# Kernel tuning notes

Hardware: AMD Instinct MI355X
Metric: run time of the kernel (lower is better)

The kernel has to match this reference:

```python
import jax, jax.numpy as jnp
import numpy as np

B, N, D, H = 4, 2048, 1024, 16
DH = D // H

def setup_inputs() -> dict:
    key = jax.random.key(0)
    kx, kqkv, ko = jax.random.split(key, 3)
    x = jax.random.normal(kx, (B, N, D), dtype=jnp.float32)
    # torch Linear weights: [out, in]; scale like default init
    W_qkv = jax.random.normal(kqkv, (3 * D, D), dtype=jnp.float32) * (1.0 / np.sqrt(D))
    W_out = jax.random.normal(ko, (D, D), dtype=jnp.float32) * (1.0 / np.sqrt(D))
    return {"x": x, "W_qkv": W_qkv, "W_out": W_out}

def reference(x, W_qkv, W_out):
    Bk, Nk, C = x.shape
    qkv = jnp.einsum('bnc,oc->bno', x, W_qkv)  # [B,N,3D]
    qkv = qkv.reshape(Bk, Nk, 3, H, DH).transpose(2, 0, 3, 1, 4)  # [3,B,H,N,DH]
    q, k, v = qkv[0], qkv[1], qkv[2]
    att = jnp.einsum('bhnd,bhmd->bhnm', q, k) * (1.0 / np.sqrt(DH))
    mask = jnp.triu(jnp.ones((Nk, Nk), dtype=bool), k=1)  # True above diagonal
    att = jnp.where(mask, -jnp.inf, att)
    att = jax.nn.softmax(att, axis=-1)
    y = jnp.einsum('bhnm,bhmd->bhnd', att, v)  # [B,H,N,DH]
    y = y.transpose(0, 2, 1, 3).reshape(Bk, Nk, C)
    return jnp.einsum('bnc,oc->bno', y, W_out)
```

## Files before the change

### kernel.cpp

```cpp
#include <hip/hip_runtime.h>
#include <hip/hip_bf16.h>
#include <stdint.h>

#define Bb 4
#define Nn 2048
#define Dd 1024
#define Hh 16
#define DHd 64
#define Mm (Bb*Nn)
#define D3 (3*Dd)

typedef unsigned short u16;
typedef unsigned int u32;
typedef __attribute__((ext_vector_type(8))) short bf16x8;
typedef __attribute__((ext_vector_type(4))) float f32x4;
typedef __attribute__((ext_vector_type(16))) float f32x16;
typedef __attribute__((ext_vector_type(4))) unsigned int u32x4;

__device__ __forceinline__ u16 f2bf(float f) {
    unsigned int u = __float_as_uint(f);
    u = (u + 0x7FFFu + ((u >> 16) & 1u)) >> 16;
    return (u16)u;
}

__device__ __forceinline__ u32 cvtpk_bf16(float lo, float hi) {
    u32 r;
    asm("v_cvt_pk_bf16_f32 %0, %1, %2" : "=v"(r) : "v"(lo), "v"(hi));
    return r;
}

__device__ __forceinline__ float fexp2(float x) {
    float r;
    asm("v_exp_f32 %0, %1" : "=v"(r) : "v"(x));
    return r;
}

#define GLOAD16(g, l)                                                          \
    __builtin_amdgcn_global_load_lds(                                          \
        (const __attribute__((address_space(1))) unsigned int*)(g),            \
        (__attribute__((address_space(3))) unsigned int*)(l), 16, 0, 0)

__global__ void cvt_all(const float* __restrict__ x, const float* __restrict__ wqkv,
                        const float* __restrict__ wout, u16* __restrict__ xb,
                        u16* __restrict__ wqkvb, u16* __restrict__ woutb, float s) {
    const int A4 = Mm * Dd / 4;
    const int B4 = D3 * Dd / 4;
    const int C4 = Dd * Dd / 4;
    const int QCUT = Dd * Dd / 4;
    const int total = A4 + B4 + C4;
    int i = blockIdx.x * blockDim.x + threadIdx.x;
    const int stride = gridDim.x * blockDim.x;
    for (; i < total; i += stride) {
        const float* src; u16* dst; int j; float sc = 1.f;
        if (i < A4) { src = x; dst = xb; j = i; }
        else if (i < A4 + B4) { j = i - A4; src = wqkv; dst = wqkvb; if (j < QCUT) sc = s; }
        else { j = i - A4 - B4; src = wout; dst = woutb; }
        float4 v = ((const float4*)src)[j];
        u16 o0 = f2bf(v.x * sc), o1 = f2bf(v.y * sc), o2 = f2bf(v.z * sc), o3 = f2bf(v.w * sc);
        ((uint2*)dst)[j] = make_uint2((u32)o0 | ((u32)o1 << 16), (u32)o2 | ((u32)o3 << 16));
    }
}

template<int OUT_F32>
__global__ __launch_bounds__(256) void gemm_bt(const u16* __restrict__ A,
                                               const u16* __restrict__ Bm,
                                               void* __restrict__ C,
                                               int M, int Nout, int K) {
    __shared__ u16 As[128 * 64];
    __shared__ u16 Bs[128 * 64];
    const int t = threadIdx.x;
    const int lane = t & 63;
    const int w = t >> 6;
    const int wr = w >> 1, wc = w & 1;
    const int l15 = lane & 15, l4 = lane >> 4;

    const int gx = gridDim.x;
    const int linear = blockIdx.y * gx + blockIdx.x;
    const int cpx = (gx * gridDim.y) >> 3;
    const int tile = (linear & 7) * cpx + (linear >> 3);
    const int m0 = (tile / gx) * 128;
    const int n0 = (tile % gx) * 128;

    f32x4 acc[4][4] = {};

    for (int k0 = 0; k0 < K; k0 += 64) {
        __syncthreads();
#pragma unroll
        for (int i = 0; i < 4; i++) {
            int chunk = i * 256 + t;
            int row = chunk >> 3;
            int csw = ((chunk & 7) ^ (row & 7)) << 3;
            GLOAD16(A + (size_t)(m0 + row) * K + k0 + csw, &As[chunk * 8]);
            GLOAD16(Bm + (size_t)(n0 + row) * K + k0 + csw, &Bs[chunk * 8]);
        }
        __syncthreads();

#pragma unroll
        for (int kh = 0; kh < 2; kh++) {
            bf16x8 a[4], b[4];
#pragma unroll
            for (int mi = 0; mi < 4; mi++) {
                int row = wr * 64 + mi * 16 + l15;
                a[mi] = *(const bf16x8*)&As[row * 64 + (((kh * 4 + l4) ^ (row & 7)) << 3)];
            }
#pragma unroll
            for (int nj = 0; nj < 4; nj++) {
                int row = wc * 64 + nj * 16 + l15;
                b[nj] = *(const bf16x8*)&Bs[row * 64 + (((kh * 4 + l4) ^ (row & 7)) << 3)];
            }
#pragma unroll
            for (int mi = 0; mi < 4; mi++)
#pragma unroll
                for (int nj = 0; nj < 4; nj++)
                    acc[mi][nj] = __builtin_amdgcn_mfma_f32_16x16x32_bf16(a[mi], b[nj], acc[mi][nj], 0, 0, 0);
        }
    }

#pragma unroll
    for (int mi = 0; mi < 4; mi++) {
#pragma unroll
        for (int nj = 0; nj < 4; nj++) {
            int col = n0 + wc * 64 + nj * 16 + l15;
#pragma unroll
            for (int r = 0; r < 4; r++) {
                int row = m0 + wr * 64 + mi * 16 + l4 * 4 + r;
                float v = acc[mi][nj][r];
                if (OUT_F32)
                    ((float*)C)[(size_t)row * Nout + col] = v;
                else
                    ((u16*)C)[(size_t)row * Nout + col] = f2bf(v);
            }
        }
    }
}

__global__ __launch_bounds__(256) void attn(const u16* __restrict__ qkv, u16* __restrict__ y) {
    __shared__ u16 SH[16384];
#define KT(b_) (SH + (b_) * 4096)
#define VT(b_) (SH + 8192 + (b_) * 4096)

    const int t = threadIdx.x;
    const int lane = t & 63;
    const int w = t >> 6;
    const int q31 = lane & 31;
    const int hi = lane >> 5;
    const int bh = blockIdx.x * 8 + (blockIdx.y & 7);
    const int qt = 15 - (int)(blockIdx.y >> 3);
    const int b = bh >> 4, h = bh & 15;

    const u16* qbase = qkv + (size_t)(b * Nn) * D3 + h * DHd;
    const u16* Kg = qbase + Dd;
    const u16* Vg = qbase + 2 * Dd;

    const int kr0 = t >> 3;
    const int ks0 = (((t & 7) ^ (kr0 & 7)) << 3);
    const int vi = t & 31;
    const int vsd = (t >> 5) * 8;
    const int vchunk = (2 * vi) >> 3;
    const int vcol = (2 * vi) & 7;

    const int q0 = qt * 128;
    const int ktmax = 2 * qt + 1;
    const int qw = q0 + w * 32;

    bf16x8 qf[4];
    {
        const u16* qrow = qbase + (size_t)(qw + q31) * D3 + hi * 8;
        qf[0] = *(const bf16x8*)(qrow);
        qf[1] = *(const bf16x8*)(qrow + 16);
        qf[2] = *(const bf16x8*)(qrow + 32);
        qf[3] = *(const bf16x8*)(qrow + 48);
    }

    f32x16 o0 = {}, o1 = {};
    float m_ = -1e30f, l_ = 0.f;
    u32x4 va, vb_;

    GLOAD16(Kg + (size_t)kr0 * D3 + ks0, KT(0) + t * 8);
    GLOAD16(Kg + (size_t)(kr0 + 32) * D3 + ks0, KT(0) + (t + 256) * 8);
    {
        const u16* vr = Vg + (size_t)(2 * vi) * D3 + vsd;
        va = *(const u32x4*)vr;
        vb_ = *(const u32x4*)(vr + D3);
    }
    asm volatile("s_waitcnt vmcnt(0)" ::: "memory");
    {
        u16 av[8], bv[8];
        *(u32x4*)av = va; *(u32x4*)bv = vb_;
#pragma unroll
        for (int j = 0; j < 8; j++) {
            int d = vsd + j;
            u32 word = (u32)av[j] | ((u32)bv[j] << 16);
            *(u32*)(VT(0) + d * 64 + ((vchunk ^ (d & 7)) << 3) + vcol) = word;
        }
    }
    __syncthreads();

    int cur = 0;
    for (int kt = 0; kt <= ktmax; ++kt) {
        const int k0 = kt * 64;
        const int havenext = (kt < ktmax);

        if (havenext) {
            const int nk0 = k0 + 64;
            GLOAD16(Kg + (size_t)(nk0 + kr0) * D3 + ks0, KT(cur ^ 1) + t * 8);
            GLOAD16(Kg + (size_t)(nk0 + kr0 + 32) * D3 + ks0, KT(cur ^ 1) + (t + 256) * 8);
            const u16* vr = Vg + (size_t)(nk0 + 2 * vi) * D3 + vsd;
            va = *(const u32x4*)vr;
            vb_ = *(const u32x4*)(vr + D3);
        }

        const int dq = qw - k0;

        if (dq >= 0) {
            const int two = (dq >= 32);

            f32x16 s0 = {}, s1 = {};
            __builtin_amdgcn_s_setprio(1);
#pragma unroll
            for (int c = 0; c < 4; ++c) {
                bf16x8 kf = *(const bf16x8*)(KT(cur) + q31 * 64 + (((2 * c + hi) ^ (q31 & 7)) << 3));
                s0 = __builtin_amdgcn_mfma_f32_32x32x16_bf16(kf, qf[c], s0, 0, 0, 0);
            }
            if (two) {
#pragma unroll
                for (int c = 0; c < 4; ++c) {
                    bf16x8 kf = *(const bf16x8*)(KT(cur) + (32 + q31) * 64 + (((2 * c + hi) ^ (q31 & 7)) << 3));
                    s1 = __builtin_amdgcn_mfma_f32_32x32x16_bf16(kf, qf[c], s1, 0, 0, 0);
                }
            }
            __builtin_amdgcn_s_setprio(0);

            if (dq == 0) {
#pragma unroll
                for (int r = 0; r < 16; ++r) {
                    int krel = (r & 3) + 8 * (r >> 2) + 4 * hi;
                    if (krel > q31) s0[r] = -1e30f;
                }
            }
            if (dq == 32) {
#pragma unroll
                for (int r = 0; r < 16; ++r) {
                    int krel = (r & 3) + 8 * (r >> 2) + 4 * hi;
                    if (krel > q31) s1[r] = -1e30f;
                }
            }

            float lm = s0[0];
#pragma unroll
            for (int r = 1; r < 16; ++r) lm = fmaxf(lm, s0[r]);
            if (two) {
#pragma unroll
                for (int r = 0; r < 16; ++r) lm = fmaxf(lm, s1[r]);
            }

            if (!__all(lm <= m_ + 8.f)) {
                float pm = __shfl_xor(lm, 32);
                float vq = fmaxf(lm, pm);
                float newm = fmaxf(m_, vq);
                float corr = fexp2(m_ - newm);
                l_ *= corr;
                o0 = o0 * corr;
                o1 = o1 * corr;
                m_ = newm;
            }

            u32 wd0[4][2], wd1[4][2];
#pragma unroll
            for (int g = 0; g < 4; ++g) {
                float p0 = fexp2(s0[4 * g + 0] - m_);
                float p1 = fexp2(s0[4 * g + 1] - m_);
                float p2 = fexp2(s0[4 * g + 2] - m_);
                float p3 = fexp2(s0[4 * g + 3] - m_);
                l_ += (p0 + p1) + (p2 + p3);
                wd0[g][0] = cvtpk_bf16(p0, p1);
                wd0[g][1] = cvtpk_bf16(p2, p3);
            }
            if (two) {
#pragma unroll
                for (int g = 0; g < 4; ++g) {
                    float p0 = fexp2(s1[4 * g + 0] - m_);
                    float p1 = fexp2(s1[4 * g + 1] - m_);
                    float p2 = fexp2(s1[4 * g + 2] - m_);
                    float p3 = fexp2(s1[4 * g + 3] - m_);
                    l_ += (p0 + p1) + (p2 + p3);
                    wd1[g][0] = cvtpk_bf16(p0, p1);
                    wd1[g][1] = cvtpk_bf16(p2, p3);
                }
            }

            __builtin_amdgcn_s_setprio(1);
#pragma unroll
            for (int c = 0; c < 2; ++c) {
                u32 a0 = wd0[2 * c][0], a1 = wd0[2 * c][1];
                u32 b0 = wd0[2 * c + 1][0], b1 = wd0[2 * c + 1][1];
                asm("v_permlane32_swap_b32 %0, %1" : "+v"(a0), "+v"(b0));
                asm("v_permlane32_swap_b32 %0, %1" : "+v"(a1), "+v"(b1));
                union { u32x4 u; bf16x8 f; } pa;
                pa.u[0] = a0; pa.u[1] = a1; pa.u[2] = b0; pa.u[3] = b1;
                bf16x8 v0 = *(const bf16x8*)(VT(cur) + q31 * 64 + (((2 * c + hi) ^ (q31 & 7)) << 3));
                bf16x8 v1 = *(const bf16x8*)(VT(cur) + (32 + q31) * 64 + (((2 * c + hi) ^ (q31 & 7)) << 3));
                o0 = __builtin_amdgcn_mfma_f32_32x32x16_bf16(v0, pa.f, o0, 0, 0, 0);
                o1 = __builtin_amdgcn_mfma_f32_32x32x16_bf16(v1, pa.f, o1, 0, 0, 0);
            }
            if (two) {
#pragma unroll
                for (int c = 0; c < 2; ++c) {
                    u32 a0 = wd1[2 * c][0], a1 = wd1[2 * c][1];
                    u32 b0 = wd1[2 * c + 1][0], b1 = wd1[2 * c + 1][1];
                    asm("v_permlane32_swap_b32 %0, %1" : "+v"(a0), "+v"(b0));
                    asm("v_permlane32_swap_b32 %0, %1" : "+v"(a1), "+v"(b1));
                    union { u32x4 u; bf16x8 f; } pa;
                    pa.u[0] = a0; pa.u[1] = a1; pa.u[2] = b0; pa.u[3] = b1;
                    int ck = 2 * (c + 2) + hi;
                    bf16x8 v0 = *(const bf16x8*)(VT(cur) + q31 * 64 + ((ck ^ (q31 & 7)) << 3));
                    bf16x8 v1 = *(const bf16x8*)(VT(cur) + (32 + q31) * 64 + ((ck ^ (q31 & 7)) << 3));
                    o0 = __builtin_amdgcn_mfma_f32_32x32x16_bf16(v0, pa.f, o0, 0, 0, 0);
                    o1 = __builtin_amdgcn_mfma_f32_32x32x16_bf16(v1, pa.f, o1, 0, 0, 0);
                }
            }
            __builtin_amdgcn_s_setprio(0);
        }

        if (havenext) {
            asm volatile("s_waitcnt vmcnt(0)" ::: "memory");
            u16 av[8], bv[8];
            *(u32x4*)av = va; *(u32x4*)bv = vb_;
#pragma unroll
            for (int j = 0; j < 8; j++) {
                int d = vsd + j;
                u32 word = (u32)av[j] | ((u32)bv[j] << 16);
                *(u32*)(VT(cur ^ 1) + d * 64 + ((vchunk ^ (d & 7)) << 3) + vcol) = word;
            }
        }
        __syncthreads();
        cur ^= 1;
    }

    float lq = l_ + __shfl_xor(l_, 32);
    float linv = 1.f / lq;
    u16* Ep = SH + w * 2304;
#pragma unroll
    for (int dt = 0; dt < 2; ++dt) {
#pragma unroll
        for (int g = 0; g < 4; ++g) {
#pragma unroll
            for (int s2 = 0; s2 < 2; ++s2) {
                float e0 = (dt ? o1[4 * g + 2 * s2] : o0[4 * g + 2 * s2]) * linv;
                float e1 = (dt ? o1[4 * g + 2 * s2 + 1] : o0[4 * g + 2 * s2 + 1]) * linv;
                u32 word = cvtpk_bf16(e0, e1);
                int chnk = 4 * dt + g;
                *(u32*)(Ep + q31 * 72 + chnk * 8 + 4 * hi + 2 * s2) = word;
            }
        }
    }
    asm volatile("s_waitcnt lgkmcnt(0)" ::: "memory");
    __builtin_amdgcn_sched_barrier(0);
    {
        int qp = lane >> 1;
        int dh = lane & 1;
        u16* yrow = y + (size_t)(b * Nn + qw + qp) * Dd + h * DHd + dh * 32;
#pragma unroll
        for (int cc = 0; cc < 4; ++cc) {
            int chnk = dh * 4 + cc;
            u32x4 vv = *(const u32x4*)(Ep + qp * 72 + chnk * 8);
            *(u32x4*)(yrow + cc * 8) = vv;
        }
    }
#undef KT
#undef VT
}

extern "C" void kernel_launch(void* const* d_in, const int* in_sizes, int n_in,
                              void* d_out, int out_size, void* d_ws, size_t ws_size,
                              hipStream_t stream) {
    const float* x = (const float*)d_in[0];
    const float* Wqkv = (const float*)d_in[1];
    const float* Wout = (const float*)d_in[2];

    char* ws = (char*)d_ws;
    size_t off = 0;
    u16* xb = (u16*)(ws + off);    off += (size_t)Mm * Dd * 2;
    u16* wqkvb = (u16*)(ws + off); off += (size_t)D3 * Dd * 2;
    u16* woutb = (u16*)(ws + off); off += (size_t)Dd * Dd * 2;
    u16* qkv = (u16*)(ws + off);   off += (size_t)Mm * D3 * 2;
    u16* yb = (u16*)(ws + off);    off += (size_t)Mm * Dd * 2;

    const float SCL = 0.125f * 1.4426950408889634f;

    cvt_all<<<4096, 256, 0, stream>>>(x, Wqkv, Wout, xb, wqkvb, woutb, SCL);

    gemm_bt<0><<<dim3(D3 / 128, Mm / 128), 256, 0, stream>>>(xb, wqkvb, qkv, Mm, D3, Dd);
    attn<<<dim3(8, 128), 256, 0, stream>>>(qkv, yb);
    gemm_bt<1><<<dim3(Dd / 128, Mm / 128), 256, 0, stream>>>(yb, woutb, d_out, Mm, Dd, Dd);
}
```

Before: 161.1 us.

## Split long causal query tiles across two blocks and merge partial softmax results

The 12 longest query tiles per head are split into two KV-range segments, each handled by a separate block. Each block writes unnormalized bf16 partial outputs plus row max and sum to workspace, and a new merge kernel combines the pairs. The goal is to even out the triangular work imbalance and shorten the tail of the attention grid. The cost is an extra kernel launch, partial-output traffic, and extra bf16 rounding of the unnormalized partials. The split path only runs when the workspace is large enough.

```diff
diff --git a/kernel.cpp b/kernel.cpp
--- a/kernel.cpp
+++ b/kernel.cpp
@@ -17,10 +17,17 @@
 typedef __attribute__((ext_vector_type(16))) float f32x16;
 typedef __attribute__((ext_vector_type(4))) unsigned int u32x4;
 
+#define REC_U16 8704
+#define WS_BASE 92274688ull
+#define WS_NEED (WS_BASE + 1536ull * REC_U16 * 2)
+
 __device__ __forceinline__ u16 f2bf(float f) {
     unsigned int u = __float_as_uint(f);
     u = (u + 0x7FFFu + ((u >> 16) & 1u)) >> 16;
     return (u16)u;
+}
+__device__ __forceinline__ float bf2f(u16 v) {
+    return __uint_as_float(((u32)v) << 16);
 }
 
 __device__ __forceinline__ u32 cvtpk_bf16(float lo, float hi) {
@@ -134,7 +141,8 @@
     }
 }
 
-__global__ __launch_bounds__(256) void attn(const u16* __restrict__ qkv, u16* __restrict__ y) {
+__global__ __launch_bounds__(256) void attn(const u16* __restrict__ qkv, u16* __restrict__ y,
+                                            u16* __restrict__ part, int split) {
     __shared__ u16 SH[16384];
 #define KT(b_) (SH + (b_) * 4096)
 #define VT(b_) (SH + 8192 + (b_) * 4096)
@@ -145,8 +153,25 @@
     const int q31 = lane & 31;
     const int hi = lane >> 5;
     const int bh = blockIdx.x * 8 + (blockIdx.y & 7);
-    const int qt = 15 - (int)(blockIdx.y >> 3);
+    const int item = blockIdx.y >> 3;
     const int b = bh >> 4, h = bh & 15;
+
+    int qt, kt_lo, kt_hi, rec = 0;
+    bool outp = false;
+    if (split) {
+        if (item < 24) {
+            qt = 15 - (item >> 1);
+            int seg = item & 1;
+            outp = true;
+            kt_lo = seg ? (qt + 1) : 0;
+            kt_hi = seg ? (2 * qt + 2) : (qt + 1);
+            rec = (bh * 12 + (15 - qt)) * 2 + seg;
+        } else {
+            qt = 27 - item; kt_lo = 0; kt_hi = 2 * qt + 2;
+        }
+    } else {
+        qt = 15 - item; kt_lo = 0; kt_hi = 2 * qt + 2;
+    }
 
     const u16* qbase = qkv + (size_t)(b * Nn) * D3 + h * DHd;
     const u16* Kg = qbase + Dd;
@@ -160,7 +185,6 @@
     const int vcol = (2 * vi) & 7;
 
     const int q0 = qt * 128;
-    const int ktmax = 2 * qt + 1;
     const int qw = q0 + w * 32;
 
     bf16x8 qf[4];
@@ -176,10 +200,11 @@
     float m_ = -1e30f, l_ = 0.f;
     u32x4 va, vb_;
 
-    GLOAD16(Kg + (size_t)kr0 * D3 + ks0, KT(0) + t * 8);
-    GLOAD16(Kg + (size_t)(kr0 + 32) * D3 + ks0, KT(0) + (t + 256) * 8);
     {
-        const u16* vr = Vg + (size_t)(2 * vi) * D3 + vsd;
+        const int k0 = kt_lo * 64;
+        GLOAD16(Kg + (size_t)(k0 + kr0) * D3 + ks0, KT(0) + t * 8);
+        GLOAD16(Kg + (size_t)(k0 + kr0 + 32) * D3 + ks0, KT(0) + (t + 256) * 8);
+        const u16* vr = Vg + (size_t)(k0 + 2 * vi) * D3 + vsd;
         va = *(const u32x4*)vr;
         vb_ = *(const u32x4*)(vr + D3);
     }
@@ -197,9 +222,9 @@
     __syncthreads();
 
     int cur = 0;
-    for (int kt = 0; kt <= ktmax; ++kt) {
+    for (int kt = kt_lo; kt < kt_hi; ++kt) {
         const int k0 = kt * 64;
-        const int havenext = (kt < ktmax);
+        const int havenext = (kt + 1 < kt_hi);
 
         if (havenext) {
             const int nk0 = k0 + 64;
@@ -338,7 +363,7 @@
     }
 
     float lq = l_ + __shfl_xor(l_, 32);
-    float linv = 1.f / lq;
+    float scl = outp ? 1.f : (1.f / lq);
     u16* Ep = SH + w * 2304;
 #pragma unroll
     for (int dt = 0; dt < 2; ++dt) {
@@ -346,8 +371,8 @@
         for (int g = 0; g < 4; ++g) {
 #pragma unroll
             for (int s2 = 0; s2 < 2; ++s2) {
-                float e0 = (dt ? o1[4 * g + 2 * s2] : o0[4 * g + 2 * s2]) * linv;
-                float e1 = (dt ? o1[4 * g + 2 * s2 + 1] : o0[4 * g + 2 * s2 + 1]) * linv;
+                float e0 = (dt ? o1[4 * g + 2 * s2] : o0[4 * g + 2 * s2]) * scl;
+                float e1 = (dt ? o1[4 * g + 2 * s2 + 1] : o0[4 * g + 2 * s2 + 1]) * scl;
                 u32 word = cvtpk_bf16(e0, e1);
                 int chnk = 4 * dt + g;
                 *(u32*)(Ep + q31 * 72 + chnk * 8 + 4 * hi + 2 * s2) = word;
@@ -359,16 +384,76 @@
     {
         int qp = lane >> 1;
         int dh = lane & 1;
-        u16* yrow = y + (size_t)(b * Nn + qw + qp) * Dd + h * DHd + dh * 32;
+        u16* dst;
+        if (outp) {
+            u16* recO = part + (size_t)rec * REC_U16;
+            dst = recO + (w * 32 + qp) * 64 + dh * 32;
+        } else {
+            dst = y + (size_t)(b * Nn + qw + qp) * Dd + h * DHd + dh * 32;
+        }
 #pragma unroll
         for (int cc = 0; cc < 4; ++cc) {
             int chnk = dh * 4 + cc;
             u32x4 vv = *(const u32x4*)(Ep + qp * 72 + chnk * 8);
-            *(u32x4*)(yrow + cc * 8) = vv;
-        }
+            *(u32x4*)(dst + cc * 8) = vv;
+        }
+    }
+    if (outp && hi == 0) {
+        u16* recO = part + (size_t)rec * REC_U16;
+        float* recM = (float*)(recO + 8192);
+        float* recL = recM + 128;
+        recM[w * 32 + q31] = m_;
+        recL[w * 32 + q31] = lq;
     }
 #undef KT
 #undef VT
+}
+
+__global__ __launch_bounds__(256) void attn_merge(const u16* __restrict__ part,
+                                                  u16* __restrict__ y) {
+    const int p = blockIdx.x;
+    const int bh = p / 12;
+    const int j = p - bh * 12;
+    const int qt = 15 - j;
+    const int b = bh >> 4, h = bh & 15;
+
+    const u16* rA = part + (size_t)(p * 2) * REC_U16;
+    const u16* rB = rA + REC_U16;
+    const float* mA = (const float*)(rA + 8192);
+    const float* lA = mA + 128;
+    const float* mB = (const float*)(rB + 8192);
+    const float* lB = mB + 128;
+
+    const int t = threadIdx.x;
+    const int row = t >> 1;
+    const int half = t & 1;
+
+    float ma = mA[row], mb = mB[row];
+    float la = lA[row], lb = lB[row];
+    float M = fmaxf(ma, mb);
+    float wa = fexp2(ma - M), wb = fexp2(mb - M);
+    float inv = 1.f / (la * wa + lb * wb);
+    wa *= inv; wb *= inv;
+
+    const u16* oa = rA + row * 64 + half * 32;
+    const u16* ob = rB + row * 64 + half * 32;
+    u16* yr = y + (size_t)(b * Nn + qt * 128 + row) * Dd + h * DHd + half * 32;
+
+#pragma unroll
+    for (int g = 0; g < 4; ++g) {
+        u32x4 ua = *(const u32x4*)(oa + g * 8);
+        u32x4 ub = *(const u32x4*)(ob + g * 8);
+        u16 av[8], bv[8];
+        *(u32x4*)av = ua; *(u32x4*)bv = ub;
+        u32 outw[4];
+#pragma unroll
+        for (int k = 0; k < 4; ++k) {
+            float v0 = bf2f(av[2 * k]) * wa + bf2f(bv[2 * k]) * wb;
+            float v1 = bf2f(av[2 * k + 1]) * wa + bf2f(bv[2 * k + 1]) * wb;
+            outw[k] = cvtpk_bf16(v0, v1);
+        }
+        *(u32x4*)(yr + g * 8) = *(u32x4*)outw;
+    }
 }
 
 extern "C" void kernel_launch(void* const* d_in, const int* in_sizes, int n_in,
@@ -385,12 +470,17 @@
     u16* woutb = (u16*)(ws + off); off += (size_t)Dd * Dd * 2;
     u16* qkv = (u16*)(ws + off);   off += (size_t)Mm * D3 * 2;
     u16* yb = (u16*)(ws + off);    off += (size_t)Mm * Dd * 2;
+    u16* part = (u16*)(ws + off);
+
+    const int split = (ws_size >= WS_NEED) ? 1 : 0;
 
     const float SCL = 0.125f * 1.4426950408889634f;
 
     cvt_all<<<4096, 256, 0, stream>>>(x, Wqkv, Wout, xb, wqkvb, woutb, SCL);
 
     gemm_bt<0><<<dim3(D3 / 128, Mm / 128), 256, 0, stream>>>(xb, wqkvb, qkv, Mm, D3, Dd);
-    attn<<<dim3(8, 128), 256, 0, stream>>>(qkv, yb);
+    attn<<<dim3(8, split ? 224 : 128), 256, 0, stream>>>(qkv, yb, part, split);
+    if (split)
+        attn_merge<<<768, 256, 0, stream>>>(part, yb);
     gemm_bt<1><<<dim3(Dd / 128, Mm / 128), 256, 0, stream>>>(yb, woutb, d_out, Mm, Dd, Dd);
 }
```

New measurement: 174.2 us. 8.1% more time.
